# Performance work log

Measured on AMD Instinct MI355X. Metric: run time of the kernel, lower is better.

Reference implementation:

```python
import jax, jax.numpy as jnp
import numpy as np

B, S, H, TOK = 64, 512, 768, 8   # batch rows, tokens/row, hidden, tokens per sentence
K = (B * S) // TOK               # 4096 sentence segments
NUM_CLASSES = 4


def setup_inputs() -> dict:
    key = jax.random.key(0)
    k0, k1, k2, k3 = jax.random.split(key, 4)
    out = jax.random.normal(k0, (B, S, H), dtype=jnp.float32)
    # each row i holds sentences i*64 .. i*64+63, 8 contiguous tokens each
    sent_ids = (jnp.arange(B * S, dtype=jnp.int64) // TOK).reshape(B, S)
    labels = jax.random.randint(k1, (B, S), 0, NUM_CLASSES, dtype=jnp.int64)
    W1 = jax.random.normal(k2, (2 * H, 512), dtype=jnp.float32) * 0.02
    b1 = jnp.zeros((512,), dtype=jnp.float32)
    W2 = jax.random.normal(k3, (512, NUM_CLASSES), dtype=jnp.float32) * 0.02
    b2 = jnp.zeros((NUM_CLASSES,), dtype=jnp.float32)
    return {"out": out, "W1": W1, "b1": b1, "W2": W2, "b2": b2,
            "labels": labels, "sent_ids": sent_ids}


def _ner_forward(out, W1, b1, W2, b2, labels, sent_ids):
    ids = sent_ids.reshape(-1)                      # [B*S]
    x = out.reshape(-1, H)                          # [B*S, H]
    n = ids.shape[0]
    valid = ids >= 0                                # -1 means padding
    seg = jnp.where(valid, ids, K).astype(jnp.int32)  # route invalid to dummy slot K
    w = valid.astype(out.dtype)

    # masked segment mean of token embeddings (avg_vector)
    counts = jax.ops.segment_sum(w, seg, num_segments=K + 1)[:K]            # [K]
    sums = jax.ops.segment_sum(x * w[:, None], seg, num_segments=K + 1)[:K]  # [K,H]
    seg_mean = sums / jnp.maximum(counts, 1.0)[:, None]

    # build_dict: cls vector of segment k = out[i][0] of LAST row containing k
    row = jnp.arange(n) // S
    cls_row = jax.ops.segment_max(jnp.where(valid, row, -1), seg, num_segments=K + 1)[:K]
    cls_vec = out[jnp.maximum(cls_row, 0), 0]       # [K, H]

    # segment label = labels[mask][0] (first token in flattened order)
    first_idx = jax.ops.segment_min(jnp.where(valid, jnp.arange(n), n), seg,
                                    num_segments=K + 1)[:K]
    seg_label = labels.reshape(-1)[jnp.minimum(first_idx, n - 1)]  # [K]

    feats = jnp.concatenate([cls_vec, seg_mean], axis=1)  # [K, 2H]
    h = jax.nn.relu(feats @ W1 + b1)                      # dropout is identity in eval
    probs = jax.nn.softmax(h @ W2 + b2, axis=1)           # [K, 4]

    # Multiclass_Focal_Loss: gather prob at label, -log, sorted truncated sum
    p = jnp.take_along_axis(probs, seg_label[:, None].astype(jnp.int32), axis=1)[:, 0]
    costs = -jnp.log(p)                                   # [K]
    pos = seg_label > 0
    Npos = jnp.sum(pos)
    neg_costs = jnp.where(seg_label == 0, costs, -jnp.inf)
    sorted_desc = -jnp.sort(-neg_costs)                   # descending
    M = jnp.floor(2.5 * Npos.astype(jnp.float32)).astype(jnp.int32)
    take = (jnp.arange(K) < M) & jnp.isfinite(sorted_desc)
    total = jnp.sum(jnp.where(pos, costs, 0.0)) + jnp.sum(jnp.where(take, sorted_desc, 0.0))
    denom = jnp.floor(3.5 * Npos.astype(jnp.float32))
    return total / denom


def reference(out, W1, b1, W2, b2, labels, sent_ids):
    return _ner_forward(out, W1, b1, W2, b2, labels, sent_ids)
```

## Files before the change

### kernel.cpp

```cpp
#include <hip/hip_runtime.h>
#include <hip/hip_bf16.h>
#include <math.h>

#define SDIM 512
#define HDIM 768
#define TOKN 8
#define KSEG 4096
#define HID 512
#define NCLS 4
#define NPANEL 16

typedef __attribute__((ext_vector_type(8))) short short8v;
typedef __attribute__((ext_vector_type(4))) float f32x4;

__device__ __forceinline__ ushort f2bf(float f) {
    union { float f; unsigned u; } x; x.f = f;
    return (ushort)((x.u + 0x7FFFu + ((x.u >> 16) & 1u)) >> 16);
}

__global__ __launch_bounds__(256) void fused_prep_k(const float* __restrict__ outp,
                                                    const float* __restrict__ W1,
                                                    ushort* __restrict__ segm,
                                                    ushort* __restrict__ W1t,
                                                    float* __restrict__ clsW,
                                                    float* __restrict__ gaccf,
                                                    unsigned* __restrict__ gcnt) {
    __shared__ float tile[32][33];
    __shared__ float cls[HDIM];
    int bid = blockIdx.x, tid = threadIdx.x;
    if (bid < KSEG) {
        if (tid >= 192) return;
        const float4* base = (const float4*)(outp + (size_t)bid * TOKN * HDIM) + tid;
        float x = 0.f, y = 0.f, z = 0.f, w = 0.f;
#pragma unroll
        for (int t = 0; t < TOKN; ++t) {
            float4 v = base[t * (HDIM / 4)];
            x += v.x; y += v.y; z += v.z; w += v.w;
        }
        ushort4 m;
        m.x = f2bf(x * 0.125f); m.y = f2bf(y * 0.125f);
        m.z = f2bf(z * 0.125f); m.w = f2bf(w * 0.125f);
        ((ushort4*)(segm + (size_t)bid * HDIM))[tid] = m;
    } else if (bid < KSEG + 384) {
        int idx = bid - KSEG;
        int k0 = (idx % 24) * 32;
        int n0 = (idx / 24) * 32;
        int tx = tid & 31, ty = tid >> 5;
#pragma unroll
        for (int i = 0; i < 4; ++i) {
            int kl = ty + i * 8;
            tile[kl][tx] = W1[(size_t)(HDIM + k0 + kl) * HID + n0 + tx];
        }
        __syncthreads();
#pragma unroll
        for (int i = 0; i < 4; ++i) {
            int nl = ty + i * 8;
            W1t[(size_t)(n0 + nl) * HDIM + k0 + tx] = f2bf(tile[tx][nl]);
        }
    } else {
        int idx = bid - (KSEG + 384);
        if (idx == 0) {
            if (tid < 2) gaccf[tid] = 0.f;
            if (tid < 3) gcnt[tid] = 0u;
        }
        int r = idx >> 1;
        int j0 = (idx & 1) << 8;
        for (int h = tid; h < HDIM; h += 256)
            cls[h] = outp[(size_t)r * SDIM * HDIM + h];
        __syncthreads();
        int j = j0 + tid;
        float a0 = 0.f, a1 = 0.f, a2 = 0.f, a3 = 0.f;
        for (int h = 0; h < HDIM; h += 4) {
            a0 = fmaf(cls[h + 0], W1[(h + 0) * HID + j], a0);
            a1 = fmaf(cls[h + 1], W1[(h + 1) * HID + j], a1);
            a2 = fmaf(cls[h + 2], W1[(h + 2) * HID + j], a2);
            a3 = fmaf(cls[h + 3], W1[(h + 3) * HID + j], a3);
        }
        clsW[r * HID + j] = (a0 + a1) + (a2 + a3);
    }
}

#define BM 64
#define BN 64
#define BKK 64

__global__ __launch_bounds__(256) void gemm_head_k(const ushort* __restrict__ A,
                                                   const ushort* __restrict__ Bt,
                                                   const float* __restrict__ clsW,
                                                   const float* __restrict__ b1,
                                                   const float* __restrict__ W2,
                                                   float* __restrict__ plog) {
    __shared__ ushort As[BM][72];
    __shared__ ushort Bs[BN][72];

    int tid = threadIdx.x, lane = tid & 63, wid = tid >> 6;
    int wm = wid >> 1, wn = wid & 1;
    int m0 = blockIdx.x * BM, n0 = blockIdx.y * BN;
    int r_a = tid >> 3, c_a = tid & 7;

    f32x4 acc[2][2] = {};
    float4 pa[2], pb[2];

#pragma unroll
    for (int i = 0; i < 2; ++i) {
        pa[i] = *(const float4*)(A  + (size_t)(m0 + r_a + 32 * i) * HDIM + c_a * 8);
        pb[i] = *(const float4*)(Bt + (size_t)(n0 + r_a + 32 * i) * HDIM + c_a * 8);
    }

    for (int kt = 0; kt < HDIM; kt += BKK) {
#pragma unroll
        for (int i = 0; i < 2; ++i) {
            *(float4*)(&As[r_a + 32 * i][c_a * 8]) = pa[i];
            *(float4*)(&Bs[r_a + 32 * i][c_a * 8]) = pb[i];
        }
        __syncthreads();
        int nkt = kt + BKK;
        if (nkt < HDIM) {
#pragma unroll
            for (int i = 0; i < 2; ++i) {
                pa[i] = *(const float4*)(A  + (size_t)(m0 + r_a + 32 * i) * HDIM + nkt + c_a * 8);
                pb[i] = *(const float4*)(Bt + (size_t)(n0 + r_a + 32 * i) * HDIM + nkt + c_a * 8);
            }
        }
        int row = lane & 15, kc = lane >> 4;
#pragma unroll
        for (int ks = 0; ks < 2; ++ks) {
            int kk = ks * 32 + kc * 8;
            short8v afrag[2], bfrag[2];
#pragma unroll
            for (int f = 0; f < 2; ++f) {
                afrag[f] = *(const short8v*)(&As[wm * 32 + f * 16 + row][kk]);
                bfrag[f] = *(const short8v*)(&Bs[wn * 32 + f * 16 + row][kk]);
            }
#pragma unroll
            for (int mf = 0; mf < 2; ++mf)
#pragma unroll
                for (int nf = 0; nf < 2; ++nf)
                    acc[mf][nf] = __builtin_amdgcn_mfma_f32_16x16x32_bf16(
                        afrag[mf], bfrag[nf], acc[mf][nf], 0, 0, 0);
        }
        __syncthreads();
    }

    int col = lane & 15, rg = lane >> 4;
    float4 w2v[2];
#pragma unroll
    for (int nf = 0; nf < 2; ++nf) {
        int gn = n0 + wn * 32 + nf * 16 + col;
        float bb = b1[gn];
        float cw = clsW[blockIdx.x * HID + gn];
        w2v[nf] = *(const float4*)(W2 + gn * 4);
#pragma unroll
        for (int mf = 0; mf < 2; ++mf)
#pragma unroll
            for (int r = 0; r < 4; ++r)
                acc[mf][nf][r] = fmaxf(acc[mf][nf][r] + cw + bb, 0.f);
    }
    int panel = blockIdx.y * 2 + wn;
#pragma unroll
    for (int c = 0; c < NCLS; ++c) {
        float w0 = (c == 0) ? w2v[0].x : (c == 1) ? w2v[0].y : (c == 2) ? w2v[0].z : w2v[0].w;
        float w1 = (c == 0) ? w2v[1].x : (c == 1) ? w2v[1].y : (c == 2) ? w2v[1].z : w2v[1].w;
        float p[2][4];
#pragma unroll
        for (int mf = 0; mf < 2; ++mf)
#pragma unroll
            for (int r = 0; r < 4; ++r)
                p[mf][r] = fmaf(acc[mf][0][r], w0, acc[mf][1][r] * w1);
#pragma unroll
        for (int off = 1; off < 16; off <<= 1)
#pragma unroll
            for (int mf = 0; mf < 2; ++mf)
#pragma unroll
                for (int r = 0; r < 4; ++r)
                    p[mf][r] += __shfl_xor(p[mf][r], off);
        if (col == 0) {
#pragma unroll
            for (int mf = 0; mf < 2; ++mf)
#pragma unroll
                for (int r = 0; r < 4; ++r) {
                    int gm = m0 + wm * 32 + mf * 16 + rg * 4 + r;
                    plog[((size_t)panel * KSEG + gm) * NCLS + c] = p[mf][r];
                }
        }
    }
}

__global__ __launch_bounds__(256) void loss_k(const float* __restrict__ plog,
                                              const float* __restrict__ b2,
                                              const int* __restrict__ labels,
                                              float* __restrict__ gaccf,
                                              unsigned* __restrict__ gcnt,
                                              float* __restrict__ negs,
                                              float* __restrict__ res) {
    __shared__ float s_p[4], s_n[4];
    __shared__ unsigned s_pc[4], s_nc[4];
    __shared__ int s_last;
    int tid = threadIdx.x, bid = blockIdx.x;
    int lane = tid & 63, wid = tid >> 6;
    float b20 = b2[0], b21 = b2[1], b22 = b2[2], b23 = b2[3];

    float psum = 0.f, nsum = 0.f;
    unsigned pcnt = 0, ncnt = 0;
#pragma unroll
    for (int i = 0; i < 2; ++i) {
        int k = bid * 512 + i * 256 + tid;
        float l0 = b20, l1 = b21, l2 = b22, l3 = b23;
#pragma unroll
        for (int pn = 0; pn < NPANEL; ++pn) {
            float4 v = *(const float4*)(plog + ((size_t)pn * KSEG + k) * NCLS);
            l0 += v.x; l1 += v.y; l2 += v.z; l3 += v.w;
        }
        int lb = labels[k * TOKN];
        float mx = fmaxf(fmaxf(l0, l1), fmaxf(l2, l3));
        float se = expf(l0 - mx) + expf(l1 - mx) + expf(l2 - mx) + expf(l3 - mx);
        float ll = (lb == 0) ? l0 : (lb == 1) ? l1 : (lb == 2) ? l2 : l3;
        float ck = logf(se) + mx - ll;
        if (lb > 0) { psum += ck; pcnt++; } else { nsum += ck; ncnt++; }
    }
#pragma unroll
    for (int off = 32; off; off >>= 1) {
        psum += __shfl_down(psum, off);
        nsum += __shfl_down(nsum, off);
        pcnt += __shfl_down(pcnt, off);
        ncnt += __shfl_down(ncnt, off);
    }
    if (lane == 0) { s_p[wid] = psum; s_n[wid] = nsum; s_pc[wid] = pcnt; s_nc[wid] = ncnt; }
    __syncthreads();
    if (tid == 0) {
        float bp = s_p[0] + s_p[1] + s_p[2] + s_p[3];
        float bn = s_n[0] + s_n[1] + s_n[2] + s_n[3];
        unsigned bpc = s_pc[0] + s_pc[1] + s_pc[2] + s_pc[3];
        unsigned bnc = s_nc[0] + s_nc[1] + s_nc[2] + s_nc[3];
        atomicAdd(&gaccf[0], bp);
        atomicAdd(&gaccf[1], bn);
        atomicAdd(&gcnt[0], bpc);
        atomicAdd(&gcnt[1], bnc);
    }
    __threadfence();
    if (tid == 0) {
        unsigned t = atomicAdd(&gcnt[2], 1u);
        s_last = (t == 7) ? 1 : 0;
    }
    __syncthreads();
    if (!s_last) return;
    __threadfence();

    float tp = __hip_atomic_load(&gaccf[0], __ATOMIC_RELAXED, __HIP_MEMORY_SCOPE_AGENT);
    float tn = __hip_atomic_load(&gaccf[1], __ATOMIC_RELAXED, __HIP_MEMORY_SCOPE_AGENT);
    unsigned np = __hip_atomic_load(&gcnt[0], __ATOMIC_RELAXED, __HIP_MEMORY_SCOPE_AGENT);
    unsigned nn = __hip_atomic_load(&gcnt[1], __ATOMIC_RELAXED, __HIP_MEMORY_SCOPE_AGENT);
    int M = (int)floorf(2.5f * (float)np);
    if ((int)nn <= M) {
        if (tid == 0) res[0] = (tp + tn) / floorf(3.5f * (float)np);
        return;
    }

    for (int k = tid; k < KSEG; k += 256) {
        float l0 = b20, l1 = b21, l2 = b22, l3 = b23;
        for (int pn = 0; pn < NPANEL; ++pn) {
            float4 v = *(const float4*)(plog + ((size_t)pn * KSEG + k) * NCLS);
            l0 += v.x; l1 += v.y; l2 += v.z; l3 += v.w;
        }
        int lb = labels[k * TOKN];
        float mx = fmaxf(fmaxf(l0, l1), fmaxf(l2, l3));
        float se = expf(l0 - mx) + expf(l1 - mx) + expf(l2 - mx) + expf(l3 - mx);
        float ll = (lb == 0) ? l0 : (lb == 1) ? l1 : (lb == 2) ? l2 : l3;
        float ck = logf(se) + mx - ll;
        negs[k] = (lb == 0) ? ck : -INFINITY;
    }
    __syncthreads();
    for (int kk = 2; kk <= KSEG; kk <<= 1) {
        for (int j = kk >> 1; j > 0; j >>= 1) {
            for (int i = tid; i < KSEG; i += 256) {
                int ixj = i ^ j;
                if (ixj > i) {
                    float a = negs[i], b = negs[ixj];
                    bool up = ((i & kk) == 0);
                    if (up ? (a > b) : (a < b)) { negs[i] = b; negs[ixj] = a; }
                }
            }
            __syncthreads();
        }
    }
    float s = 0.f;
    for (int i = tid; i < M; i += 256) {
        float v = negs[KSEG - 1 - i];
        if (isfinite(v)) s += v;
    }
#pragma unroll
    for (int off = 32; off; off >>= 1) s += __shfl_down(s, off);
    if (lane == 0) s_p[wid] = s;
    __syncthreads();
    if (tid == 0) {
        float t = s_p[0] + s_p[1] + s_p[2] + s_p[3];
        res[0] = (tp + t) / floorf(3.5f * (float)np);
    }
}

extern "C" void kernel_launch(void* const* d_in, const int* in_sizes, int n_in,
                              void* d_out, int out_size, void* d_ws, size_t ws_size,
                              hipStream_t stream) {
    const float* outp   = (const float*)d_in[0];
    const float* W1     = (const float*)d_in[1];
    const float* b1     = (const float*)d_in[2];
    const float* W2     = (const float*)d_in[3];
    const float* b2     = (const float*)d_in[4];
    const int*   labels = (const int*)d_in[5];

    char* ws = (char*)d_ws;
    ushort*   segm  = (ushort*)ws;
    ushort*   W1t   = (ushort*)(ws + 6291456);
    float*    clsW  = (float*) (ws + 7077888);
    float*    plog  = (float*) (ws + 7208960);
    float*    negs  = (float*) (ws + 8257536);
    float*    gaccf = (float*) (ws + 8273920);
    unsigned* gcnt  = (unsigned*)(ws + 8273928);
    float*    res   = (float*)d_out;

    fused_prep_k<<<KSEG + 384 + 128, 256, 0, stream>>>(outp, W1, segm, W1t, clsW,
                                                       gaccf, gcnt);
    gemm_head_k<<<dim3(KSEG / BM, HID / BN), 256, 0, stream>>>(
        segm, W1t, clsW, b1, W2, plog);
    loss_k<<<8, 256, 0, stream>>>(plog, b2, labels, gaccf, gcnt, negs, res);
}
```

Before: 77.46 us.

## Compute CLS projection with MFMA blocks and pack four segments per mean block

The CLS-vector projection (64 rows × 768 × first half of W1), previously done by 128 blocks of scalar FMA, now runs in 8 blocks that convert the data to bf16 and use MFMA 16x16x32 tiles. These blocks are placed first in the grid so the long-running work is scheduled early. The segment-mean part now handles four segments per 256-thread block (1024 blocks instead of 4096 with a quarter of the threads idle), which cuts block count and raises thread utilisation. The CLS projection now uses bf16 precision instead of fp32, which adds rounding error.

```diff
diff --git a/kernel.cpp b/kernel.cpp
--- a/kernel.cpp
+++ b/kernel.cpp
@@ -25,24 +25,76 @@
                                                     float* __restrict__ clsW,
                                                     float* __restrict__ gaccf,
                                                     unsigned* __restrict__ gcnt) {
-    __shared__ float tile[32][33];
-    __shared__ float cls[HDIM];
+    __shared__ __align__(16) char smem[18432];
     int bid = blockIdx.x, tid = threadIdx.x;
-    if (bid < KSEG) {
-        if (tid >= 192) return;
-        const float4* base = (const float4*)(outp + (size_t)bid * TOKN * HDIM) + tid;
-        float x = 0.f, y = 0.f, z = 0.f, w = 0.f;
-#pragma unroll
-        for (int t = 0; t < TOKN; ++t) {
-            float4 v = base[t * (HDIM / 4)];
-            x += v.x; y += v.y; z += v.z; w += v.w;
-        }
-        ushort4 m;
-        m.x = f2bf(x * 0.125f); m.y = f2bf(y * 0.125f);
-        m.z = f2bf(z * 0.125f); m.w = f2bf(w * 0.125f);
-        ((ushort4*)(segm + (size_t)bid * HDIM))[tid] = m;
-    } else if (bid < KSEG + 384) {
-        int idx = bid - KSEG;
+
+    if (bid < 8) {
+        ushort (*As)[72] = (ushort(*)[72])smem;
+        ushort (*Bs)[72] = (ushort(*)[72])(smem + 9216);
+        if (bid == 0) {
+            if (tid < 2) gaccf[tid] = 0.f;
+            if (tid < 3) gcnt[tid] = 0u;
+        }
+        int nc = bid * 64;
+        int lane = tid & 63, wid = tid >> 6;
+        int wm = wid >> 1, wn = wid & 1;
+        f32x4 acc[2][2] = {};
+        int am = tid >> 2, aq = tid & 3;
+        int bk = tid >> 4, bq = tid & 15;
+        for (int kt = 0; kt < HDIM; kt += 64) {
+#pragma unroll
+            for (int i = 0; i < 4; ++i) {
+                int k = aq * 16 + i * 4;
+                float4 v = *(const float4*)(outp + (size_t)am * SDIM * HDIM + kt + k);
+                ushort4 u;
+                u.x = f2bf(v.x); u.y = f2bf(v.y); u.z = f2bf(v.z); u.w = f2bf(v.w);
+                *(ushort4*)(&As[am][k]) = u;
+            }
+#pragma unroll
+            for (int i = 0; i < 4; ++i) {
+                int krow = bk + i * 16;
+                int n4 = bq * 4;
+                float4 v = *(const float4*)(W1 + (size_t)(kt + krow) * HID + nc + n4);
+                Bs[n4 + 0][krow] = f2bf(v.x);
+                Bs[n4 + 1][krow] = f2bf(v.y);
+                Bs[n4 + 2][krow] = f2bf(v.z);
+                Bs[n4 + 3][krow] = f2bf(v.w);
+            }
+            __syncthreads();
+            int row = lane & 15, kc = lane >> 4;
+#pragma unroll
+            for (int ks = 0; ks < 2; ++ks) {
+                int kk = ks * 32 + kc * 8;
+                short8v afrag[2], bfrag[2];
+#pragma unroll
+                for (int f = 0; f < 2; ++f) {
+                    afrag[f] = *(const short8v*)(&As[wm * 32 + f * 16 + row][kk]);
+                    bfrag[f] = *(const short8v*)(&Bs[wn * 32 + f * 16 + row][kk]);
+                }
+#pragma unroll
+                for (int mf = 0; mf < 2; ++mf)
+#pragma unroll
+                    for (int nf = 0; nf < 2; ++nf)
+                        acc[mf][nf] = __builtin_amdgcn_mfma_f32_16x16x32_bf16(
+                            afrag[mf], bfrag[nf], acc[mf][nf], 0, 0, 0);
+            }
+            __syncthreads();
+        }
+        int col = lane & 15, rg = lane >> 4;
+#pragma unroll
+        for (int mf = 0; mf < 2; ++mf)
+#pragma unroll
+            for (int nf = 0; nf < 2; ++nf) {
+                int gn = nc + wn * 32 + nf * 16 + col;
+#pragma unroll
+                for (int r = 0; r < 4; ++r) {
+                    int gm = wm * 32 + mf * 16 + rg * 4 + r;
+                    clsW[gm * HID + gn] = acc[mf][nf][r];
+                }
+            }
+    } else if (bid < 8 + 384) {
+        float (*tile)[33] = (float(*)[33])smem;
+        int idx = bid - 8;
         int k0 = (idx % 24) * 32;
         int n0 = (idx / 24) * 32;
         int tx = tid & 31, ty = tid >> 5;
@@ -58,25 +110,25 @@
             W1t[(size_t)(n0 + nl) * HDIM + k0 + tx] = f2bf(tile[tx][nl]);
         }
     } else {
-        int idx = bid - (KSEG + 384);
-        if (idx == 0) {
-            if (tid < 2) gaccf[tid] = 0.f;
-            if (tid < 3) gcnt[tid] = 0u;
-        }
-        int r = idx >> 1;
-        int j0 = (idx & 1) << 8;
-        for (int h = tid; h < HDIM; h += 256)
-            cls[h] = outp[(size_t)r * SDIM * HDIM + h];
-        __syncthreads();
-        int j = j0 + tid;
-        float a0 = 0.f, a1 = 0.f, a2 = 0.f, a3 = 0.f;
-        for (int h = 0; h < HDIM; h += 4) {
-            a0 = fmaf(cls[h + 0], W1[(h + 0) * HID + j], a0);
-            a1 = fmaf(cls[h + 1], W1[(h + 1) * HID + j], a1);
-            a2 = fmaf(cls[h + 2], W1[(h + 2) * HID + j], a2);
-            a3 = fmaf(cls[h + 3], W1[(h + 3) * HID + j], a3);
-        }
-        clsW[r * HID + j] = (a0 + a1) + (a2 + a3);
+        int s0 = (bid - 392) * 4;
+#pragma unroll
+        for (int i = 0; i < 3; ++i) {
+            int o = tid + i * 256;
+            int s4 = o / 192;
+            int c  = o % 192;
+            const float4* base = (const float4*)outp +
+                                 (size_t)(s0 + s4) * (TOKN * HDIM / 4) + c;
+            float x = 0.f, y = 0.f, z = 0.f, w = 0.f;
+#pragma unroll
+            for (int t = 0; t < TOKN; ++t) {
+                float4 v = base[t * (HDIM / 4)];
+                x += v.x; y += v.y; z += v.z; w += v.w;
+            }
+            ushort4 m;
+            m.x = f2bf(x * 0.125f); m.y = f2bf(y * 0.125f);
+            m.z = f2bf(z * 0.125f); m.w = f2bf(w * 0.125f);
+            ((ushort4*)(segm + (size_t)(s0 + s4) * HDIM))[c] = m;
+        }
     }
 }
 
@@ -318,8 +370,8 @@
     unsigned* gcnt  = (unsigned*)(ws + 8273928);
     float*    res   = (float*)d_out;
 
-    fused_prep_k<<<KSEG + 384 + 128, 256, 0, stream>>>(outp, W1, segm, W1t, clsW,
-                                                       gaccf, gcnt);
+    fused_prep_k<<<8 + 384 + 1024, 256, 0, stream>>>(outp, W1, segm, W1t, clsW,
+                                                     gaccf, gcnt);
     gemm_head_k<<<dim3(KSEG / BM, HID / BN), 256, 0, stream>>>(
         segm, W1t, clsW, b1, W2, plog);
     loss_k<<<8, 256, 0, stream>>>(plog, b2, labels, gaccf, gcnt, negs, res);
```

Result: faster. 70.83 us (-8.6%).
